# Performance work log

Hardware: AMD Instinct MI355X
Metric: run time of the kernel (lower is better)

## Reference

```python
import jax, jax.numpy as jnp
import numpy as np

EPS = 1e-05
QN, QP = -128.0, 127.0


def setup_inputs() -> dict:
    key = jax.random.key(0)
    kx, kw = jax.random.split(key)
    x = jax.random.normal(kx, (4, 2048, 4096), dtype=jnp.float32)
    weight = jax.random.normal(kw, (4096, 4096), dtype=jnp.float32)  # [out, in]
    return {"x": x, "weight": weight}


def reference(x, weight):
    # --- per-token int8 activation quantization (activation_quant) ---
    # s: [B, S, 1], scale so that max(|x|) maps to 127
    s = QP / jnp.clip(jnp.max(jnp.abs(x), axis=-1, keepdims=True), 1e-05, None)
    q = jnp.clip(jnp.round(x * s), QN, QP)  # int8-valued, kept in float
    xq = q / s  # dequantized activations fed to the matmul

    # --- ternary weight quantization (terniarize + pack/unpack round-trip) ---
    scale_w = 1.0 / jnp.clip(jnp.mean(jnp.abs(weight)), EPS, None)
    tw = jnp.clip(jnp.round(weight * scale_w), -1.0, 1.0)  # ternary {-1,0,1}, [out, in]

    # --- bitmat: (xq) @ tw^T, then dequant by weight scale ---
    out = jnp.einsum('bsi,oi->bso', xq, tw) / scale_w
    return out
```

## Files before the change

### kernel.cpp

```cpp
#include <hip/hip_runtime.h>
#include <stdint.h>

#define K_DIM 4096
#define M_TOK 8192
#define N_OUT 4096

typedef int v4i __attribute__((ext_vector_type(4)));


#define BAR()                                     \
    do {                                          \
        asm volatile("" ::: "memory");            \
        __builtin_amdgcn_s_barrier();             \
        asm volatile("" ::: "memory");            \
    } while (0)

__device__ __forceinline__ void gload_lds16(const void* g, void* l) {
    auto gp = reinterpret_cast<const __attribute__((address_space(1))) uint32_t*>(
        reinterpret_cast<uintptr_t>(g));
    auto lp = reinterpret_cast<__attribute__((address_space(3))) uint32_t*>(
        reinterpret_cast<uintptr_t>(l));
    __builtin_amdgcn_global_load_lds(gp, lp, 16, 0, 0);
}

__global__ __launch_bounds__(256) void quant_act(const float* __restrict__ x,
                                                 int8_t* __restrict__ q,
                                                 float* __restrict__ rs,
                                                 double* __restrict__ acc) {
    const int token = blockIdx.x;
    const int t = threadIdx.x;
    if (token == 0 && t == 0) *acc = 0.0;
    const float4* x4 = (const float4*)(x + (size_t)token * K_DIM);
    float4 v[4];
    float m = 0.0f;
#pragma unroll
    for (int r = 0; r < 4; ++r) {
        v[r] = x4[t + 256 * r];
        m = fmaxf(m, fmaxf(fmaxf(fabsf(v[r].x), fabsf(v[r].y)),
                           fmaxf(fabsf(v[r].z), fabsf(v[r].w))));
    }
#pragma unroll
    for (int off = 32; off; off >>= 1) m = fmaxf(m, __shfl_down(m, off, 64));
    __shared__ float wmax[4];
    __shared__ float smax;
    if ((t & 63) == 0) wmax[t >> 6] = m;
    __syncthreads();
    if (t == 0) smax = fmaxf(fmaxf(wmax[0], wmax[1]), fmaxf(wmax[2], wmax[3]));
    __syncthreads();
    const float s = 127.0f / fmaxf(smax, 1e-5f);
    char4* q4 = (char4*)(q + (size_t)token * K_DIM);
#pragma unroll
    for (int r = 0; r < 4; ++r) {
        float4 f = v[r];
        char4 c;
        c.x = (signed char)fminf(fmaxf(rintf(f.x * s), -128.0f), 127.0f);
        c.y = (signed char)fminf(fmaxf(rintf(f.y * s), -128.0f), 127.0f);
        c.z = (signed char)fminf(fmaxf(rintf(f.z * s), -128.0f), 127.0f);
        c.w = (signed char)fminf(fmaxf(rintf(f.w * s), -128.0f), 127.0f);
        q4[t + 256 * r] = c;
    }
    if (t == 0) rs[token] = 1.0f / s;
}

__global__ __launch_bounds__(256) void wabs_sum(const float* __restrict__ w,
                                                double* __restrict__ acc) {
    const size_t n4 = (size_t)N_OUT * K_DIM / 4;
    const size_t stride = (size_t)gridDim.x * 256;
    const float4* w4 = (const float4*)w;
    float sum = 0.0f;
    for (size_t j = (size_t)blockIdx.x * 256 + threadIdx.x; j < n4; j += stride) {
        float4 f = w4[j];
        sum += fabsf(f.x) + fabsf(f.y) + fabsf(f.z) + fabsf(f.w);
    }
    double d = (double)sum;
#pragma unroll
    for (int off = 32; off; off >>= 1) d += __shfl_down(d, off, 64);
    __shared__ double wsum[4];
    const int t = threadIdx.x;
    if ((t & 63) == 0) wsum[t >> 6] = d;
    __syncthreads();
    if (t == 0) atomicAdd(acc, wsum[0] + wsum[1] + wsum[2] + wsum[3]);
}

__global__ __launch_bounds__(256) void ternarize(const float* __restrict__ w,
                                                 int8_t* __restrict__ tw,
                                                 const double* __restrict__ acc) {
    const double mean = *acc * (1.0 / ((double)N_OUT * (double)K_DIM));
    const float sw = 1.0f / fmaxf((float)mean, 1e-5f);
    const size_t i = (size_t)blockIdx.x * 256 + threadIdx.x;
    const float4* w4 = (const float4*)w;
    char4* t4 = (char4*)tw;
    float4 f = w4[i];
    char4 c;
    c.x = (signed char)fminf(fmaxf(rintf(f.x * sw), -1.0f), 1.0f);
    c.y = (signed char)fminf(fmaxf(rintf(f.y * sw), -1.0f), 1.0f);
    c.z = (signed char)fminf(fmaxf(rintf(f.z * sw), -1.0f), 1.0f);
    c.w = (signed char)fminf(fmaxf(rintf(f.w * sw), -1.0f), 1.0f);
    t4[i] = c;
}

__global__ __launch_bounds__(512, 2) void gemm_i8(const int8_t* __restrict__ A,
                                                  const int8_t* __restrict__ B,
                                                  const float* __restrict__ rs,
                                                  const double* __restrict__ acc,
                                                  float* __restrict__ out) {
    const int nwgx = N_OUT / 256;
    const int orig = blockIdx.y * nwgx + blockIdx.x;
    const int wg = (orig & 7) * 64 + (orig >> 3);
    const int bm = (wg / nwgx) * 256;
    const int bn = (wg % nwgx) * 256;

    __shared__ int8_t smem[4][2][16384];

    const int t0 = threadIdx.x;
    const int lane = t0 & 63;
    const int wave = t0 >> 6;
    const int wm = (wave >> 1) * 64;
    const int wn = (wave & 1) * 128;

    v4i accv[4][8] = {};

    const int R0 = t0 >> 2;
    const int scol = (((t0 & 3) ^ (R0 & 3) ^ ((R0 >> 2) & 3)) << 4);
    const int8_t* Ag = A + (size_t)(bm + R0) * K_DIM + scol;
    const int8_t* Bg = B + (size_t)(bn + R0) * K_DIM + scol;
    int8_t* ldst = &smem[0][0][0] + (size_t)t0 * 16;

    const int fr = lane & 15;
    const int co = (((lane >> 4) ^ (fr & 3) ^ (fr >> 2)) << 4);

#pragma unroll
    for (int pt = 0; pt < 3; ++pt) {
        const int k0 = pt * 64;
        int8_t* sb = ldst + pt * 32768;
        gload_lds16(Ag + k0, sb);
        gload_lds16(Ag + k0 + (size_t)128 * K_DIM, sb + 8192);
        gload_lds16(Bg + k0, sb + 16384);
        gload_lds16(Bg + k0 + (size_t)128 * K_DIM, sb + 24576);
    }
    asm volatile("s_waitcnt vmcnt(8)" ::: "memory");
    BAR();

#pragma unroll 1
    for (int t = 0; t < 64; ++t) {
        const int slot = t & 3;
        const int8_t* aB = &smem[slot][0][0];
        const int8_t* bB = &smem[slot][1][0];
        const bool st = (t < 61);
        const int ks = (t + 3) * 64;
        int8_t* sb = ldst + ((t + 3) & 3) * 32768;

        v4i af[4];
#pragma unroll
        for (int p = 0; p < 4; ++p) {
            if (p == 0) {
#pragma unroll
                for (int i = 0; i < 4; ++i)
                    af[i] = *(const v4i*)(aB + (wm + i * 16 + fr) * 64 + co);
            }
            v4i b0 = *(const v4i*)(bB + (wn + (2 * p) * 16 + fr) * 64 + co);
            v4i b1 = *(const v4i*)(bB + (wn + (2 * p + 1) * 16 + fr) * 64 + co);
            if (st) {
                if (p == 0) gload_lds16(Ag + ks, sb);
                else if (p == 1) gload_lds16(Ag + ks + (size_t)128 * K_DIM, sb + 8192);
                else if (p == 2) gload_lds16(Bg + ks, sb + 16384);
                else gload_lds16(Bg + ks + (size_t)128 * K_DIM, sb + 24576);
            }
            BAR();
            __builtin_amdgcn_s_setprio(1);
#pragma unroll
            for (int i = 0; i < 4; ++i) {
                accv[i][2 * p] = __builtin_amdgcn_mfma_i32_16x16x64_i8(af[i], b0, accv[i][2 * p], 0, 0, 0);
                accv[i][2 * p + 1] = __builtin_amdgcn_mfma_i32_16x16x64_i8(af[i], b1, accv[i][2 * p + 1], 0, 0, 0);
            }
            __builtin_amdgcn_s_setprio(0);
            if (p < 3) BAR();
        }
        if (t < 61) asm volatile("s_waitcnt vmcnt(8)" ::: "memory");
        else if (t == 61) asm volatile("s_waitcnt vmcnt(4)" ::: "memory");
        else if (t == 62) asm volatile("s_waitcnt vmcnt(0)" ::: "memory");
        if (t < 63) BAR();
    }

    const double mean = *acc * (1.0 / ((double)N_OUT * (double)K_DIM));
    const float wmean = fmaxf((float)mean, 1e-5f);
    const int crow0 = (lane >> 4) * 4;
    const int ccol = lane & 15;
#pragma unroll
    for (int i = 0; i < 4; ++i) {
        const int rbase = bm + wm + i * 16 + crow0;
#pragma unroll
        for (int reg = 0; reg < 4; ++reg) {
            const int r = rbase + reg;
            const float scale = rs[r] * wmean;
            float* orow = out + (size_t)r * N_OUT + bn + wn + ccol;
#pragma unroll
            for (int j = 0; j < 8; ++j)
                orow[j * 16] = (float)accv[i][j][reg] * scale;
        }
    }
}

extern "C" void kernel_launch(void* const* d_in, const int* in_sizes, int n_in,
                              void* d_out, int out_size, void* d_ws, size_t ws_size,
                              hipStream_t stream) {
    const float* x = (const float*)d_in[0];
    const float* w = (const float*)d_in[1];
    float* out = (float*)d_out;
    char* ws = (char*)d_ws;
    int8_t* q = (int8_t*)ws;
    int8_t* tw = (int8_t*)(ws + 33554432);
    float* rs = (float*)(ws + 50331648);
    double* acc = (double*)(ws + 50364416);

    hipLaunchKernelGGL(quant_act, dim3(M_TOK), dim3(256), 0, stream, x, q, rs, acc);
    hipLaunchKernelGGL(wabs_sum, dim3(1024), dim3(256), 0, stream, w, acc);
    hipLaunchKernelGGL(ternarize, dim3((N_OUT * (size_t)K_DIM / 4) / 256), dim3(256), 0, stream, w, tw, acc);
    hipLaunchKernelGGL(gemm_i8, dim3(N_OUT / 256, M_TOK / 256), dim3(512), 0, stream, q, tw, rs, acc, out);
}
```

Before: 415.6 us.

## Switch int8 GEMM to 32x32x32 MFMA tiles with two k-substeps

Replaces the 16x16x64 int8 MFMA with the 32x32x32 variant, so each wave computes a 64x128 tile as 2x4 32x32 blocks. Each 64-wide k slab is split into two 32-wide substeps, which halves the barriers per iteration and changes the LDS fragment reads and swizzle indexing. The epilogue is rewritten for the 32x32 accumulator layout. Larger MFMA tiles need fewer fragment loads per FLOP but change register pressure and can introduce LDS bank conflicts with the existing swizzle.

```diff
diff --git a/kernel.cpp b/kernel.cpp
--- a/kernel.cpp
+++ b/kernel.cpp
@@ -6,6 +6,7 @@
 #define N_OUT 4096
 
 typedef int v4i __attribute__((ext_vector_type(4)));
+typedef int v16i __attribute__((ext_vector_type(16)));
 
 
 #define BAR()                                     \
@@ -118,7 +119,7 @@
     const int wm = (wave >> 1) * 64;
     const int wn = (wave & 1) * 128;
 
-    v4i accv[4][8] = {};
+    v16i accv[2][4] = {};
 
     const int R0 = t0 >> 2;
     const int scol = (((t0 & 3) ^ (R0 & 3) ^ ((R0 >> 2) & 3)) << 4);
@@ -126,8 +127,9 @@
     const int8_t* Bg = B + (size_t)(bn + R0) * K_DIM + scol;
     int8_t* ldst = &smem[0][0][0] + (size_t)t0 * 16;
 
-    const int fr = lane & 15;
-    const int co = (((lane >> 4) ^ (fr & 3) ^ (fr >> 2)) << 4);
+    const int l31 = lane & 31;
+    const int lh = lane >> 5;
+    const int sx = (l31 & 3) ^ ((l31 >> 2) & 3);
 
 #pragma unroll
     for (int pt = 0; pt < 3; ++pt) {
@@ -147,34 +149,36 @@
         const int8_t* aB = &smem[slot][0][0];
         const int8_t* bB = &smem[slot][1][0];
         const bool st = (t < 61);
-        const int ks = (t + 3) * 64;
+        const int ksg = (t + 3) * 64;
         int8_t* sb = ldst + ((t + 3) & 3) * 32768;
 
-        v4i af[4];
-#pragma unroll
-        for (int p = 0; p < 4; ++p) {
-            if (p == 0) {
-#pragma unroll
-                for (int i = 0; i < 4; ++i)
-                    af[i] = *(const v4i*)(aB + (wm + i * 16 + fr) * 64 + co);
-            }
-            v4i b0 = *(const v4i*)(bB + (wn + (2 * p) * 16 + fr) * 64 + co);
-            v4i b1 = *(const v4i*)(bB + (wn + (2 * p + 1) * 16 + fr) * 64 + co);
+#pragma unroll
+        for (int ks = 0; ks < 2; ++ks) {
+            const int co = (((ks * 2 + lh) ^ sx) << 4);
+            v4i af0 = *(const v4i*)(aB + (wm + l31) * 64 + co);
+            v4i af1 = *(const v4i*)(aB + (wm + 32 + l31) * 64 + co);
+            v4i bf[4];
+#pragma unroll
+            for (int n = 0; n < 4; ++n)
+                bf[n] = *(const v4i*)(bB + (wn + n * 32 + l31) * 64 + co);
             if (st) {
-                if (p == 0) gload_lds16(Ag + ks, sb);
-                else if (p == 1) gload_lds16(Ag + ks + (size_t)128 * K_DIM, sb + 8192);
-                else if (p == 2) gload_lds16(Bg + ks, sb + 16384);
-                else gload_lds16(Bg + ks + (size_t)128 * K_DIM, sb + 24576);
+                if (ks == 0) {
+                    gload_lds16(Ag + ksg, sb);
+                    gload_lds16(Ag + ksg + (size_t)128 * K_DIM, sb + 8192);
+                } else {
+                    gload_lds16(Bg + ksg, sb + 16384);
+                    gload_lds16(Bg + ksg + (size_t)128 * K_DIM, sb + 24576);
+                }
             }
             BAR();
             __builtin_amdgcn_s_setprio(1);
 #pragma unroll
-            for (int i = 0; i < 4; ++i) {
-                accv[i][2 * p] = __builtin_amdgcn_mfma_i32_16x16x64_i8(af[i], b0, accv[i][2 * p], 0, 0, 0);
-                accv[i][2 * p + 1] = __builtin_amdgcn_mfma_i32_16x16x64_i8(af[i], b1, accv[i][2 * p + 1], 0, 0, 0);
+            for (int n = 0; n < 4; ++n) {
+                accv[0][n] = __builtin_amdgcn_mfma_i32_32x32x32_i8(af0, bf[n], accv[0][n], 0, 0, 0);
+                accv[1][n] = __builtin_amdgcn_mfma_i32_32x32x32_i8(af1, bf[n], accv[1][n], 0, 0, 0);
             }
             __builtin_amdgcn_s_setprio(0);
-            if (p < 3) BAR();
+            if (ks == 0) BAR();
         }
         if (t < 61) asm volatile("s_waitcnt vmcnt(8)" ::: "memory");
         else if (t == 61) asm volatile("s_waitcnt vmcnt(4)" ::: "memory");
@@ -184,19 +188,16 @@
 
     const double mean = *acc * (1.0 / ((double)N_OUT * (double)K_DIM));
     const float wmean = fmaxf((float)mean, 1e-5f);
-    const int crow0 = (lane >> 4) * 4;
-    const int ccol = lane & 15;
-#pragma unroll
-    for (int i = 0; i < 4; ++i) {
-        const int rbase = bm + wm + i * 16 + crow0;
-#pragma unroll
-        for (int reg = 0; reg < 4; ++reg) {
-            const int r = rbase + reg;
-            const float scale = rs[r] * wmean;
-            float* orow = out + (size_t)r * N_OUT + bn + wn + ccol;
-#pragma unroll
-            for (int j = 0; j < 8; ++j)
-                orow[j * 16] = (float)accv[i][j][reg] * scale;
+#pragma unroll
+    for (int m = 0; m < 2; ++m) {
+#pragma unroll
+        for (int r = 0; r < 16; ++r) {
+            const int row = bm + wm + m * 32 + (r & 3) + 8 * (r >> 2) + 4 * lh;
+            const float scale = rs[row] * wmean;
+            float* orow = out + (size_t)row * N_OUT + bn + wn + l31;
+#pragma unroll
+            for (int n = 0; n < 4; ++n)
+                orow[n * 32] = (float)accv[m][n][r] * scale;
         }
     }
 }
```

Measured after the change: 410.6 us. About the same (-1.2%).
